# Optimization experiments

Hardware: AMD Instinct MI355X
Metric: run time of the kernel (lower is better)

## Reference

```python
import jax, jax.numpy as jnp
import numpy as np


def haar_dwt2(x):
    """Single-level 2D Haar DWT on last two axes, matching pywt.dwt2('haar').

    x: [..., H, W] with H, W even.
    Returns [..., 4, H/2, W/2] stacked as (LL, LH, HL, HH) where, per pywt,
    LH=cH (highpass along H, lowpass along W), HL=cV, HH=cD.
    """
    B, C, H, W = x.shape
    # group 2x2 blocks: [B, C, H/2, 2, W/2, 2]
    xb = x.reshape(B, C, H // 2, 2, W // 2, 2)
    x00 = xb[:, :, :, 0, :, 0]  # even row, even col
    x01 = xb[:, :, :, 0, :, 1]  # even row, odd col
    x10 = xb[:, :, :, 1, :, 0]  # odd row, even col
    x11 = xb[:, :, :, 1, :, 1]  # odd row, odd col
    half = jnp.asarray(0.5, dtype=x.dtype)
    LL = (x00 + x01 + x10 + x11) * half
    LH = (x00 + x01 - x10 - x11) * half  # cH: detail along rows (H)
    HL = (x00 - x01 + x10 - x11) * half  # cV: detail along cols (W)
    HH = (x00 - x01 - x10 + x11) * half  # cD: detail both axes
    return jnp.stack([LL, LH, HL, HH], axis=1)  # [B, 4, C, H/2, W/2]


def setup_inputs() -> dict:
    key = jax.random.key(0)
    x = jax.random.normal(key, (8, 32, 512, 512), dtype=jnp.float32)
    return {"input": x}


def reference(input):
    return haar_dwt2(input)
```

## Files before the change

kernel.cpp:

```cpp
#include <hip/hip_runtime.h>


#define B_   8
#define C_   32
#define H2_  256
#define W2_  256
#define WPAIRS_ (W2_/2)

__global__ __launch_bounds__(256)
void WaveletTransform_14319420965150_kernel(const float* __restrict__ x,
                                            float* __restrict__ out) {
    int tid = blockIdx.x * blockDim.x + threadIdx.x;
    int wp = tid & (WPAIRS_ - 1);
    int h2 = (tid >> 7) & (H2_ - 1);
    int c  = (tid >> 15) & (C_ - 1);
    int b  = tid >> 20;

    const float4* row0 = (const float4*)(x + ((((size_t)b * C_ + c) * 512 + 2 * h2) * 512));
    const float4* row1 = row0 + (512 / 4);
    float4 t = row0[wp];
    float4 u = row1[wp];

    float2 LL, LH, HL, HH;
    {
        float s0 = t.x + t.y, d0 = t.x - t.y;
        float s1 = u.x + u.y, d1 = u.x - u.y;
        LL.x = (s0 + s1) * 0.5f;
        LH.x = (s0 - s1) * 0.5f;
        HL.x = (d0 + d1) * 0.5f;
        HH.x = (d0 - d1) * 0.5f;
    }
    {
        float s0 = t.z + t.w, d0 = t.z - t.w;
        float s1 = u.z + u.w, d1 = u.z - u.w;
        LL.y = (s0 + s1) * 0.5f;
        LH.y = (s0 - s1) * 0.5f;
        HL.y = (d0 + d1) * 0.5f;
        HH.y = (d0 - d1) * 0.5f;
    }

    float2* o = (float2*)out;
    size_t obase = (((size_t)b * 4) * C_ + c) * (H2_ * W2_ / 2)
                 + (size_t)h2 * (W2_ / 2) + wp;
    const size_t qstride = (size_t)C_ * (H2_ * W2_ / 2);
    o[obase]               = LL;
    o[obase +     qstride] = LH;
    o[obase + 2 * qstride] = HL;
    o[obase + 3 * qstride] = HH;
}

extern "C" void kernel_launch(void* const* d_in, const int* in_sizes, int n_in,
                              void* d_out, int out_size, void* d_ws, size_t ws_size,
                              hipStream_t stream) {
    const float* x = (const float*)d_in[0];
    float* out = (float*)d_out;
    const int total = B_ * C_ * H2_ * WPAIRS_;
    const int block = 256;
    const int grid = total / block;
    WaveletTransform_14319420965150_kernel<<<grid, block, 0, stream>>>(x, out);
}
```

Baseline: 431.8 us.

## Widen per-thread work to float4 stores with nontemporal writes and grid-stride loop

Each thread now processes four output columns per row pair, loading four 16-byte vectors and writing 16-byte vectors to each subband instead of 8-byte ones. Output stores use nontemporal hints to avoid polluting cache with write-once data. The launch switches to a fixed 2048-block grid-stride loop. This is meant to raise effective memory bandwidth. The risks are lower occupancy-driven parallelism and the loop overhead.

```diff
diff --git a/kernel.cpp b/kernel.cpp
--- a/kernel.cpp
+++ b/kernel.cpp
@@ -5,48 +5,56 @@
 #define C_   32
 #define H2_  256
 #define W2_  256
-#define WPAIRS_ (W2_/2)
+#define WQ_  (W2_/4)
+
+typedef float v4f __attribute__((ext_vector_type(4)));
 
 __global__ __launch_bounds__(256)
 void WaveletTransform_14319420965150_kernel(const float* __restrict__ x,
                                             float* __restrict__ out) {
-    int tid = blockIdx.x * blockDim.x + threadIdx.x;
-    int wp = tid & (WPAIRS_ - 1);
-    int h2 = (tid >> 7) & (H2_ - 1);
-    int c  = (tid >> 15) & (C_ - 1);
-    int b  = tid >> 20;
+    const int total  = B_ * C_ * H2_ * WQ_;
+    const int stride = gridDim.x * blockDim.x;
 
-    const float4* row0 = (const float4*)(x + ((((size_t)b * C_ + c) * 512 + 2 * h2) * 512));
-    const float4* row1 = row0 + (512 / 4);
-    float4 t = row0[wp];
-    float4 u = row1[wp];
+    const v4f* __restrict__ xin = (const v4f*)x;
+    v4f* __restrict__ o         = (v4f*)out;
+    const size_t qstride = (size_t)C_ * (H2_ * W2_ / 4);
 
-    float2 LL, LH, HL, HH;
-    {
-        float s0 = t.x + t.y, d0 = t.x - t.y;
-        float s1 = u.x + u.y, d1 = u.x - u.y;
-        LL.x = (s0 + s1) * 0.5f;
-        LH.x = (s0 - s1) * 0.5f;
-        HL.x = (d0 + d1) * 0.5f;
-        HH.x = (d0 - d1) * 0.5f;
+    for (int tid = blockIdx.x * blockDim.x + threadIdx.x; tid < total; tid += stride) {
+        const int wq = tid & (WQ_ - 1);
+        const int h2 = (tid >> 6) & (H2_ - 1);
+        const int bc = tid >> 14;
+
+        const size_t r0 = ((size_t)bc * 512 + 2 * h2) * (512 / 4) + 2 * wq;
+        v4f t0 = xin[r0];
+        v4f t1 = xin[r0 + 1];
+        v4f u0 = xin[r0 + 128];
+        v4f u1 = xin[r0 + 129];
+
+        v4f LL, LH, HL, HH;
+        { float s0 = t0.x + t0.y, d0 = t0.x - t0.y;
+          float s1 = u0.x + u0.y, d1 = u0.x - u0.y;
+          LL.x = (s0 + s1) * 0.5f; LH.x = (s0 - s1) * 0.5f;
+          HL.x = (d0 + d1) * 0.5f; HH.x = (d0 - d1) * 0.5f; }
+        { float s0 = t0.z + t0.w, d0 = t0.z - t0.w;
+          float s1 = u0.z + u0.w, d1 = u0.z - u0.w;
+          LL.y = (s0 + s1) * 0.5f; LH.y = (s0 - s1) * 0.5f;
+          HL.y = (d0 + d1) * 0.5f; HH.y = (d0 - d1) * 0.5f; }
+        { float s0 = t1.x + t1.y, d0 = t1.x - t1.y;
+          float s1 = u1.x + u1.y, d1 = u1.x - u1.y;
+          LL.z = (s0 + s1) * 0.5f; LH.z = (s0 - s1) * 0.5f;
+          HL.z = (d0 + d1) * 0.5f; HH.z = (d0 - d1) * 0.5f; }
+        { float s0 = t1.z + t1.w, d0 = t1.z - t1.w;
+          float s1 = u1.z + u1.w, d1 = u1.z - u1.w;
+          LL.w = (s0 + s1) * 0.5f; LH.w = (s0 - s1) * 0.5f;
+          HL.w = (d0 + d1) * 0.5f; HH.w = (d0 - d1) * 0.5f; }
+
+        const size_t ob = ((size_t)(bc >> 5) * (4 * C_) + (bc & (C_ - 1))) * (H2_ * W2_ / 4)
+                        + (size_t)h2 * (W2_ / 4) + wq;
+        __builtin_nontemporal_store(LL, &o[ob]);
+        __builtin_nontemporal_store(LH, &o[ob +     qstride]);
+        __builtin_nontemporal_store(HL, &o[ob + 2 * qstride]);
+        __builtin_nontemporal_store(HH, &o[ob + 3 * qstride]);
     }
-    {
-        float s0 = t.z + t.w, d0 = t.z - t.w;
-        float s1 = u.z + u.w, d1 = u.z - u.w;
-        LL.y = (s0 + s1) * 0.5f;
-        LH.y = (s0 - s1) * 0.5f;
-        HL.y = (d0 + d1) * 0.5f;
-        HH.y = (d0 - d1) * 0.5f;
-    }
-
-    float2* o = (float2*)out;
-    size_t obase = (((size_t)b * 4) * C_ + c) * (H2_ * W2_ / 2)
-                 + (size_t)h2 * (W2_ / 2) + wp;
-    const size_t qstride = (size_t)C_ * (H2_ * W2_ / 2);
-    o[obase]               = LL;
-    o[obase +     qstride] = LH;
-    o[obase + 2 * qstride] = HL;
-    o[obase + 3 * qstride] = HH;
 }
 
 extern "C" void kernel_launch(void* const* d_in, const int* in_sizes, int n_in,
@@ -54,8 +62,7 @@
                               hipStream_t stream) {
     const float* x = (const float*)d_in[0];
     float* out = (float*)d_out;
-    const int total = B_ * C_ * H2_ * WPAIRS_;
     const int block = 256;
-    const int grid = total / block;
+    const int grid  = 2048;
     WaveletTransform_14319420965150_kernel<<<grid, block, 0, stream>>>(x, out);
 }
```

Measured after the change: 449.6 us. 4.1% more time.
